# Kernel tuning notes

Measured on AMD Instinct MI355X. Metric: run time of the kernel, lower is better.

Reference implementation:

```python
import jax, jax.numpy as jnp
import numpy as np

N = 262144          # batch size
C = 100             # num_classes
R0, R1 = 0.95, 1.0  # recall_range
LAM = 0.5           # lambda_pauc
LS = 0.1            # label_smoothing
MAX_PAUC = R1 - R0


def setup_inputs() -> dict:
    key = jax.random.key(0)
    k1, k2 = jax.random.split(key)
    predictions = jax.random.normal(k1, (N, C), dtype=jnp.float32)
    targets = jax.random.randint(k2, (N,), 0, C)
    weight = jnp.ones((C,), dtype=jnp.float32)
    return {"predictions": predictions, "targets": targets, "weight": weight}


def _roc_curves(scores, labels):
    """Vectorized per-class ROC. scores, labels: [C, N].
    Replaces the O(N^2) per-threshold loop with sort + cumsum (tie-correct:
    tp at threshold s_j counts ALL samples with score >= s_j)."""
    order = jnp.argsort(-scores, axis=1)                      # descending
    ss = jnp.take_along_axis(scores, order, axis=1)           # [C, N]
    sl = jnp.take_along_axis(labels, order, axis=1)           # [C, N]
    cpos = jnp.cumsum(sl, axis=1)                             # cumulative positives
    # last index within each tie-group of equal scores
    neg = -ss  # ascending
    idx = jax.vmap(lambda a: jnp.searchsorted(a, a, side='right'))(neg) - 1
    tp = jnp.take_along_axis(cpos, idx, axis=1)
    cnt = (idx + 1).astype(scores.dtype)
    fp = cnt - tp
    P = cpos[:, -1:]                       # total positives per class
    Nn = scores.shape[1] - P               # total negatives per class
    tpr = jnp.where(P > 0, tp / jnp.maximum(P, 1.0), 0.0)
    fpr = jnp.where(Nn > 0, fp / jnp.maximum(Nn, 1.0), 0.0)
    return fpr, tpr


def reference(predictions, targets, weight):
    probs = jax.nn.softmax(predictions, axis=1)               # [N, C]
    onehot = jnp.eye(C, dtype=predictions.dtype)[targets]     # [N, C]
    onehot_s = (1.0 - LS) * onehot + LS / C

    # per-class binary labels (smoothed true-class value > 0.5)
    labels = (onehot_s > 0.5).astype(predictions.dtype).T     # [C, N]
    scores = probs.T                                          # [C, N]

    fpr, tpr = _roc_curves(scores, labels)
    mask = (tpr >= R0) & (tpr <= R1)
    y = jnp.maximum(tpr - R0, 0.0)
    # tpr is monotone non-decreasing, so the recall mask is contiguous and
    # trapz over the masked subset == sum over adjacent pairs both in mask.
    pm = (mask[:, :-1] & mask[:, 1:]).astype(predictions.dtype)
    pauc = jnp.sum(0.5 * (y[:, :-1] + y[:, 1:]) * (fpr[:, 1:] - fpr[:, :-1]) * pm, axis=1)  # [C]

    avg_p_auc = jnp.sum(pauc * weight) / (jnp.sum(weight) * MAX_PAUC)
    # torch computes TP/FP via .item(): the pAUC path carries no gradient
    avg_p_auc = jax.lax.stop_gradient(jnp.clip(avg_p_auc, 0.0, 1.0))

    log_probs = jax.nn.log_softmax(predictions, axis=1)
    ce_loss = -jnp.mean(jnp.sum(onehot_s * log_probs * weight, axis=1))
    pauc_loss = 1.0 - avg_p_auc ** 2
    return (1.0 - LAM) * ce_loss + LAM * pauc_loss
```

## Files before the change

kernel.cpp:

```cpp
#include <hip/hip_runtime.h>
#include <math.h>

#define WAVE 64
constexpr int   CC      = 100;
constexpr int   MAXM    = 160;
constexpr int   BUCKET  = 4096;
constexpr int   LCAP    = 4096;
constexpr float LSMOOTH = 0.1f;
constexpr int   TILE    = 64;
constexpr int   ZN      = 3 * CC + 8;

__global__ __launch_bounds__(256) void k1_tile(
    const float* __restrict__ pred, const int* __restrict__ targets,
    const float* __restrict__ weight, float* __restrict__ L_out,
    float* __restrict__ pos_out, float* __restrict__ ce_partial,
    int* __restrict__ zero_blk, int N)
{
    __shared__ float tile[TILE * CC];
    __shared__ int   ttgt[TILE];
    __shared__ float tL[TILE], tpos[TILE];
    __shared__ float cered[4];
    const int tid = threadIdx.x;
    const int r0  = blockIdx.x * TILE;

    if (blockIdx.x == 0)
        for (int i = tid; i < ZN; i += 256) zero_blk[i] = 0;

    const float4* src = (const float4*)(pred + (size_t)r0 * CC);
    #pragma unroll
    for (int t = tid; t < TILE * (CC / 4); t += 256)
        *((float4*)&tile[t * 4]) = src[t];
    if (tid < TILE) ttgt[tid] = targets[r0 + tid];
    __syncthreads();

    const int x = tid & 15;
    const int G = tid >> 4;
    float w[7];
    #pragma unroll
    for (int j = 0; j < 7; ++j) {
        int c = x + 16 * j;
        w[j] = (c < CC) ? weight[c] : 0.0f;
    }
    float Wl = 0.0f;
    #pragma unroll
    for (int j = 0; j < 7; ++j) Wl += w[j];
    #pragma unroll
    for (int off = 1; off < 16; off <<= 1) Wl += __shfl_xor(Wl, off, 16);

    float ce_acc = 0.0f;
    #pragma unroll
    for (int rr = 0; rr < 4; ++rr) {
        const int r = G * 4 + rr;
        const float* rp = tile + r * CC;
        float v[7];
        #pragma unroll
        for (int j = 0; j < 7; ++j) {
            int c = x + 16 * j;
            v[j] = (c < CC) ? rp[c] : -INFINITY;
        }
        float vmax = v[0];
        #pragma unroll
        for (int j = 1; j < 7; ++j) vmax = fmaxf(vmax, v[j]);
        #pragma unroll
        for (int off = 1; off < 16; off <<= 1) vmax = fmaxf(vmax, __shfl_xor(vmax, off, 16));
        float z = 0.0f, ws = 0.0f;
        #pragma unroll
        for (int j = 0; j < 7; ++j) {
            int c = x + 16 * j;
            if (c < CC) { z += __expf(v[j] - vmax); ws += w[j] * v[j]; }
        }
        #pragma unroll
        for (int off = 1; off < 16; off <<= 1) {
            z  += __shfl_xor(z,  off, 16);
            ws += __shfl_xor(ws, off, 16);
        }
        float L = vmax + __logf(z);
        if (x == 0) {
            int t = ttgt[r];
            float pt = rp[t];
            tL[r] = L; tpos[r] = pt - L;
            ce_acc += -((1.0f - LSMOOTH) * weight[t] * (pt - L)
                        + (LSMOOTH / CC) * (ws - Wl * L));
        }
    }
    #pragma unroll
    for (int off = 32; off; off >>= 1) ce_acc += __shfl_xor(ce_acc, off, WAVE);
    if ((tid & 63) == 0) cered[tid >> 6] = ce_acc;
    __syncthreads();
    if (tid < TILE) {
        L_out[r0 + tid]   = tL[tid];
        pos_out[r0 + tid] = tpos[tid];
    }
    if (tid == 0)
        ce_partial[blockIdx.x] = cered[0] + cered[1] + cered[2] + cered[3];
}

__global__ __launch_bounds__(256) void k1b_scatter(
    const int* __restrict__ targets, const float* __restrict__ pos,
    int* __restrict__ cls_cnt, float* __restrict__ bucket, int N)
{
    __shared__ int hist[CC];
    __shared__ int base[CC];
    __shared__ int loc[CC];
    const int tid = threadIdx.x;
    const int rowsPerBlock = N / gridDim.x;
    const int r0 = blockIdx.x * rowsPerBlock;
    const int r1 = r0 + rowsPerBlock;
    for (int c = tid; c < CC; c += blockDim.x) { hist[c] = 0; loc[c] = 0; }
    __syncthreads();
    for (int r = r0 + tid; r < r1; r += blockDim.x)
        atomicAdd(&hist[targets[r]], 1);
    __syncthreads();
    for (int c = tid; c < CC; c += blockDim.x)
        base[c] = (hist[c] > 0) ? atomicAdd(&cls_cnt[c], hist[c]) : 0;
    __syncthreads();
    for (int r = r0 + tid; r < r1; r += blockDim.x) {
        int c = targets[r];
        int idx = base[c] + atomicAdd(&loc[c], 1);
        if (idx < BUCKET) bucket[(size_t)c * BUCKET + idx] = pos[r];
    }
}

__global__ __launch_bounds__(256) void k2_select(
    const float* __restrict__ bucket, const int* __restrict__ cls_cnt,
    float* __restrict__ u, int* __restrict__ m_arr, int* __restrict__ P_arr,
    float* __restrict__ wm_arr)
{
    __shared__ unsigned int keys[BUCKET];
    __shared__ unsigned int hist[256];
    __shared__ unsigned int scan[256];
    __shared__ unsigned int sel[256];
    __shared__ unsigned int s_prefix;
    __shared__ int s_rank;
    __shared__ int cnt_lt;
    const int c   = blockIdx.x;
    const int tid = threadIdx.x;
    const int P = min(cls_cnt[c], BUCKET);
    double Kd = 0.95 * (double)P;
    int kf = (int)floor(Kd);
    int m = P - kf;
    if (m > MAXM) m = MAXM;
    if (m < 0) m = 0;
    if (tid == 0) {
        m_arr[c] = m; P_arr[c] = P;
        wm_arr[c] = (float)((double)(kf + 1) - Kd);
        s_prefix = 0; s_rank = m - 1; cnt_lt = 0;
    }
    for (int i = tid; i < P; i += 256) {
        unsigned int b = __float_as_uint(bucket[(size_t)c * BUCKET + i]);
        keys[i] = (b & 0x80000000u) ? ~b : (b | 0x80000000u);
    }
    __syncthreads();
    if (m == 0) return;

    for (int shift = 24; shift >= 0; shift -= 8) {
        hist[tid] = 0;
        __syncthreads();
        unsigned int pref = s_prefix;
        for (int i = tid; i < P; i += 256) {
            unsigned int k = keys[i];
            bool match = (shift == 24) || ((k >> (shift + 8)) == pref);
            if (match) atomicAdd(&hist[(k >> shift) & 255u], 1u);
        }
        __syncthreads();
        scan[tid] = hist[tid];
        __syncthreads();
        for (int off = 1; off < 256; off <<= 1) {
            unsigned int add = (tid >= off) ? scan[tid - off] : 0u;
            __syncthreads();
            scan[tid] += add;
            __syncthreads();
        }
        int r = s_rank;
        unsigned int inc = scan[tid];
        unsigned int exc = inc - hist[tid];
        __syncthreads();
        if ((unsigned int)r >= exc && (unsigned int)r < inc) {
            s_rank   = r - (int)exc;
            s_prefix = (pref << 8) | (unsigned int)tid;
        }
        __syncthreads();
    }
    const unsigned int kth = s_prefix;

    for (int i = tid; i < P; i += 256) {
        unsigned int k = keys[i];
        if (k < kth) {
            int pslot = atomicAdd(&cnt_lt, 1);
            sel[pslot] = k;
        }
    }
    __syncthreads();
    const int nlt = cnt_lt;
    for (int j = nlt + tid; j < 256; j += 256) sel[j] = (j < m) ? kth : 0xFFFFFFFFu;
    __syncthreads();
    for (int kk = 2; kk <= 256; kk <<= 1) {
        for (int j = kk >> 1; j > 0; j >>= 1) {
            int i = tid, ixj = tid ^ j;
            if (ixj > i) {
                unsigned int a = sel[i], b = sel[ixj];
                bool up = ((i & kk) == 0);
                if ((a > b) == up) { sel[i] = b; sel[ixj] = a; }
            }
            __syncthreads();
        }
    }
    if (tid < m) {
        unsigned int k = sel[tid];
        unsigned int b = (k & 0x80000000u) ? (k & 0x7fffffffu) : ~k;
        u[c * MAXM + tid] = __uint_as_float(b);
    }
}

__device__ __forceinline__ int ubound(const float* uc, int m, float key, int maxidx) {
    int l = 0;
    #pragma unroll
    for (int s = 128; s; s >>= 1) {
        int p = l + s - 1;
        float val = uc[p < maxidx ? p : maxidx];
        l += ((p < m) && (val <= key)) ? s : 0;
    }
    return l;
}

__global__ __launch_bounds__(256) void k3_fused(
    const float4* __restrict__ pred4, const float* __restrict__ L,
    const float* __restrict__ u, const int* __restrict__ m_arr,
    int* __restrict__ g_cnt, int* __restrict__ g_sum, int* __restrict__ done,
    const float* __restrict__ ce_partial, int nPartial,
    const float* __restrict__ weight, const int* __restrict__ P_arr,
    const float* __restrict__ wm_arr, float* __restrict__ out,
    int N, int total4)
{
    __shared__ float umax_s[CC];
    __shared__ int   sm[CC];
    __shared__ int   lcnt[CC], lsum[CC];
    __shared__ uint2 buf[LCAP];
    __shared__ int   lc;
    __shared__ int   isLast;
    __shared__ double r1[256], r2[256], r3[256];
    const int tid = threadIdx.x;
    if (tid < CC) {
        int m = m_arr[tid];
        sm[tid] = m;
        umax_s[tid] = (m > 0) ? u[tid * MAXM + m - 1] : -INFINITY;
        lcnt[tid] = 0; lsum[tid] = 0;
    }
    if (tid == 0) lc = 0;
    __syncthreads();

    const int stride = gridDim.x * blockDim.x;
    int i = blockIdx.x * blockDim.x + tid;
    int j = i % 25;
    int n = i / 25;
    const int dj = stride % 25, dn = stride / 25;
    while (i < total4) {
        float4 v = pred4[i];
        float Ln = L[n];
        float4 um = *((const float4*)&umax_s[j * 4]);
        float s0 = v.x - Ln, s1 = v.y - Ln, s2 = v.z - Ln, s3 = v.w - Ln;
        #pragma unroll
        for (int q = 0; q < 4; ++q) {
            float sc = (q == 0) ? s0 : (q == 1) ? s1 : (q == 2) ? s2 : s3;
            float mx = (q == 0) ? um.x : (q == 1) ? um.y : (q == 2) ? um.z : um.w;
            if (sc < mx) {
                int c = j * 4 + q;
                int idx = atomicAdd(&lc, 1);
                if (idx < LCAP) {
                    buf[idx] = make_uint2((unsigned int)c, __float_as_uint(sc));
                } else {
                    int m = sm[c];
                    int l = ubound(u + c * MAXM, m, sc, MAXM - 1);
                    atomicAdd(&lcnt[c], 1);
                    atomicAdd(&lsum[c], m - 1 - l);
                }
            }
        }
        i += stride; j += dj; n += dn;
        if (j >= 25) { j -= 25; n += 1; }
    }
    __syncthreads();

    const int cnt = min(lc, LCAP);
    for (int k = tid; k < cnt; k += 256) {
        uint2 e = buf[k];
        int c = (int)e.x;
        float key = __uint_as_float(e.y);
        int m = sm[c];
        int l = ubound(u + c * MAXM, m, key, MAXM - 1);
        atomicAdd(&lcnt[c], 1);
        atomicAdd(&lsum[c], m - 1 - l);
    }
    __syncthreads();
    for (int c = tid; c < CC; c += 256) {
        if (lcnt[c]) { atomicAdd(&g_cnt[c], lcnt[c]); atomicAdd(&g_sum[c], lsum[c]); }
    }

    if (tid == 0) {
        __threadfence();
        int t = atomicAdd(done, 1);
        isLast = (t == (int)gridDim.x - 1);
    }
    __syncthreads();
    if (!isLast) return;
    __threadfence();

    double ce = 0.0;
    for (int k = tid; k < nPartial; k += 256) ce += (double)ce_partial[k];
    double p = 0.0, wsum = 0.0;
    for (int c = tid; c < CC; c += 256) {
        int P = P_arr[c], m = sm[c];
        double wgt = (double)weight[c];
        long long Nn = (long long)N - P;
        if (P > 0 && Nn > 0 && m > 0) {
            double wm = (double)wm_arr[c];
            double S   = (double)atomicAdd(&g_sum[c], 0)
                       + wm * (double)atomicAdd(&g_cnt[c], 0);
            double sub = 0.5 * (double)(m - 1) * (double)(m - 2) + wm * (double)(m - 1);
            double pc  = (S - sub) / ((double)Nn * (double)P);
            if (pc < 0.0) pc = 0.0;
            p += pc * wgt;
        }
        wsum += wgt;
    }
    r1[tid] = ce; r2[tid] = p; r3[tid] = wsum;
    __syncthreads();
    for (int off = 128; off; off >>= 1) {
        if (tid < off) {
            r1[tid] += r1[tid + off];
            r2[tid] += r2[tid + off];
            r3[tid] += r3[tid + off];
        }
        __syncthreads();
    }
    if (tid == 0) {
        double ce_loss = r1[0] / (double)N;
        double avg = r2[0] / (r3[0] * 0.05);
        avg = fmin(fmax(avg, 0.0), 1.0);
        out[0] = (float)(0.5 * ce_loss + 0.5 * (1.0 - avg * avg));
    }
}

extern "C" void kernel_launch(void* const* d_in, const int* in_sizes, int n_in,
                              void* d_out, int out_size, void* d_ws, size_t ws_size,
                              hipStream_t stream) {
    (void)n_in; (void)out_size; (void)ws_size;
    const float* pred    = (const float*)d_in[0];
    const int*   targets = (const int*)d_in[1];
    const float* weight  = (const float*)d_in[2];
    float* out = (float*)d_out;
    const int N = in_sizes[1];

    const int K1_BLOCKS = N / TILE;
    char* base = (char*)d_ws;
    size_t off = 0;
    auto take = [&](size_t bytes) { char* q = base + off; off += (bytes + 15) & ~(size_t)15; return q; };
    float* L_ws       = (float*)take((size_t)N * 4);
    float* pos_ws     = (float*)take((size_t)N * 4);
    float* ce_partial = (float*)take((size_t)K1_BLOCKS * 4);
    float* u          = (float*)take((size_t)CC * MAXM * 4);
    int*   m_arr      = (int*)take(CC * 4);
    int*   P_arr      = (int*)take(CC * 4);
    float* wm_arr     = (float*)take(CC * 4);
    int*   zero_blk   = (int*)take(ZN * 4);
    int*   cls_cnt  = zero_blk;
    int*   g_cnt    = zero_blk + CC;
    int*   g_sum    = zero_blk + 2 * CC;
    int*   done     = zero_blk + 3 * CC;
    float* bucket     = (float*)take((size_t)CC * BUCKET * 4);

    k1_tile<<<K1_BLOCKS, 256, 0, stream>>>(pred, targets, weight, L_ws, pos_ws,
                                           ce_partial, zero_blk, N);
    k1b_scatter<<<256, 256, 0, stream>>>(targets, pos_ws, cls_cnt, bucket, N);
    k2_select<<<CC, 256, 0, stream>>>(bucket, cls_cnt, u, m_arr, P_arr, wm_arr);
    const int total4 = (int)((size_t)N * CC / 4);
    k3_fused<<<1024, 256, 0, stream>>>((const float4*)pred, L_ws, u, m_arr,
                                       g_cnt, g_sum, done, ce_partial, K1_BLOCKS,
                                       weight, P_arr, wm_arr, out, N, total4);
}
```

Baseline: 265.5 us.

## Reduce k3 per-block pAUC partials directly and double grid with smaller LDS buffer

Each k3 block now computes its weighted pAUC contribution locally and writes one double partial to a per-block slot, instead of atomically adding per-class counts into global counters. The last block sums the partials and subtracts a per-class correction term. The double reduction arrays now reuse the candidate buffer, and LCAP is halved, which shrinks shared memory per block; the grid doubles to 2048 blocks so more blocks can be resident. This trades fewer global atomics and better occupancy against a larger final reduction and a greater chance of overflowing the smaller per-block candidate buffer.

Result: no change. 267.2 us (+0.6%).

```diff
diff --git a/kernel.cpp b/kernel.cpp
--- a/kernel.cpp
+++ b/kernel.cpp
@@ -5,10 +5,11 @@
 constexpr int   CC      = 100;
 constexpr int   MAXM    = 160;
 constexpr int   BUCKET  = 4096;
-constexpr int   LCAP    = 4096;
+constexpr int   LCAP    = 2048;
 constexpr float LSMOOTH = 0.1f;
 constexpr int   TILE    = 64;
-constexpr int   ZN      = 3 * CC + 8;
+constexpr int   ZN      = CC + 8;
+constexpr int   K3_BLOCKS = 2048;
 
 __global__ __launch_bounds__(256) void k1_tile(
     const float* __restrict__ pred, const int* __restrict__ targets,
@@ -226,23 +227,27 @@
 __global__ __launch_bounds__(256) void k3_fused(
     const float4* __restrict__ pred4, const float* __restrict__ L,
     const float* __restrict__ u, const int* __restrict__ m_arr,
-    int* __restrict__ g_cnt, int* __restrict__ g_sum, int* __restrict__ done,
+    const int* __restrict__ P_arr, const float* __restrict__ wm_arr,
+    const float* __restrict__ weight,
+    unsigned long long* __restrict__ partial_p, int* __restrict__ done,
     const float* __restrict__ ce_partial, int nPartial,
-    const float* __restrict__ weight, const int* __restrict__ P_arr,
-    const float* __restrict__ wm_arr, float* __restrict__ out,
-    int N, int total4)
+    float* __restrict__ out, int N, int total4)
 {
     __shared__ float umax_s[CC];
     __shared__ int   sm[CC];
+    __shared__ int   sP[CC];
+    __shared__ float swm[CC], swgt[CC];
     __shared__ int   lcnt[CC], lsum[CC];
     __shared__ uint2 buf[LCAP];
     __shared__ int   lc;
     __shared__ int   isLast;
-    __shared__ double r1[256], r2[256], r3[256];
     const int tid = threadIdx.x;
     if (tid < CC) {
         int m = m_arr[tid];
-        sm[tid] = m;
+        sm[tid]  = m;
+        sP[tid]  = P_arr[tid];
+        swm[tid] = wm_arr[tid];
+        swgt[tid] = weight[tid];
         umax_s[tid] = (m > 0) ? u[tid * MAXM + m - 1] : -INFINITY;
         lcnt[tid] = 0; lsum[tid] = 0;
     }
@@ -292,9 +297,25 @@
         atomicAdd(&lsum[c], m - 1 - l);
     }
     __syncthreads();
-    for (int c = tid; c < CC; c += 256) {
-        if (lcnt[c]) { atomicAdd(&g_cnt[c], lcnt[c]); atomicAdd(&g_sum[c], lsum[c]); }
-    }
+
+    double part = 0.0;
+    if (tid < CC) {
+        int P = sP[tid], m = sm[tid];
+        if (P > 0 && P < N && m > 0) {
+            part = (double)swgt[tid]
+                 * ((double)lsum[tid] + (double)swm[tid] * (double)lcnt[tid])
+                 / ((double)(N - P) * (double)P);
+        }
+    }
+    double* red = (double*)buf;
+    red[tid] = part;
+    __syncthreads();
+    for (int off = 128; off; off >>= 1) {
+        if (tid < off) red[tid] += red[tid + off];
+        __syncthreads();
+    }
+    if (tid == 0)
+        atomicExch(&partial_p[blockIdx.x], (unsigned long long)__double_as_longlong(red[0]));
 
     if (tid == 0) {
         __threadfence();
@@ -305,37 +326,41 @@
     if (!isLast) return;
     __threadfence();
 
+    double psum = 0.0;
+    for (int b = tid; b < (int)gridDim.x; b += 256)
+        psum += __longlong_as_double((long long)atomicAdd(&partial_p[b], 0ull));
     double ce = 0.0;
     for (int k = tid; k < nPartial; k += 256) ce += (double)ce_partial[k];
-    double p = 0.0, wsum = 0.0;
-    for (int c = tid; c < CC; c += 256) {
-        int P = P_arr[c], m = sm[c];
-        double wgt = (double)weight[c];
-        long long Nn = (long long)N - P;
-        if (P > 0 && Nn > 0 && m > 0) {
-            double wm = (double)wm_arr[c];
-            double S   = (double)atomicAdd(&g_sum[c], 0)
-                       + wm * (double)atomicAdd(&g_cnt[c], 0);
-            double sub = 0.5 * (double)(m - 1) * (double)(m - 2) + wm * (double)(m - 1);
-            double pc  = (S - sub) / ((double)Nn * (double)P);
-            if (pc < 0.0) pc = 0.0;
-            p += pc * wgt;
-        }
-        wsum += wgt;
-    }
-    r1[tid] = ce; r2[tid] = p; r3[tid] = wsum;
+    double sub = 0.0, wsum = 0.0;
+    if (tid < CC) {
+        wsum = (double)swgt[tid];
+        int P = sP[tid], m = sm[tid];
+        if (P > 0 && P < N && m > 0) {
+            double wm = (double)swm[tid];
+            sub = (double)swgt[tid]
+                * (0.5 * (double)(m - 1) * (double)(m - 2) + wm * (double)(m - 1))
+                / ((double)(N - P) * (double)P);
+        }
+    }
+    __syncthreads();
+    double* r1 = red; double* r2 = red + 256;
+    r1[tid] = ce; r2[tid] = psum - sub;
     __syncthreads();
     for (int off = 128; off; off >>= 1) {
-        if (tid < off) {
-            r1[tid] += r1[tid + off];
-            r2[tid] += r2[tid + off];
-            r3[tid] += r3[tid + off];
-        }
+        if (tid < off) { r1[tid] += r1[tid + off]; r2[tid] += r2[tid + off]; }
+        __syncthreads();
+    }
+    double ce_tot = r1[0], p_tot = r2[0];
+    __syncthreads();
+    r1[tid] = wsum;
+    __syncthreads();
+    for (int off = 128; off; off >>= 1) {
+        if (tid < off) r1[tid] += r1[tid + off];
         __syncthreads();
     }
     if (tid == 0) {
-        double ce_loss = r1[0] / (double)N;
-        double avg = r2[0] / (r3[0] * 0.05);
+        double ce_loss = ce_tot / (double)N;
+        double avg = p_tot / (r1[0] * 0.05);
         avg = fmin(fmax(avg, 0.0), 1.0);
         out[0] = (float)(0.5 * ce_loss + 0.5 * (1.0 - avg * avg));
     }
@@ -364,9 +389,8 @@
     float* wm_arr     = (float*)take(CC * 4);
     int*   zero_blk   = (int*)take(ZN * 4);
     int*   cls_cnt  = zero_blk;
-    int*   g_cnt    = zero_blk + CC;
-    int*   g_sum    = zero_blk + 2 * CC;
-    int*   done     = zero_blk + 3 * CC;
+    int*   done     = zero_blk + CC;
+    unsigned long long* partial_p = (unsigned long long*)take((size_t)K3_BLOCKS * 8);
     float* bucket     = (float*)take((size_t)CC * BUCKET * 4);
 
     k1_tile<<<K1_BLOCKS, 256, 0, stream>>>(pred, targets, weight, L_ws, pos_ws,
@@ -374,7 +398,7 @@
     k1b_scatter<<<256, 256, 0, stream>>>(targets, pos_ws, cls_cnt, bucket, N);
     k2_select<<<CC, 256, 0, stream>>>(bucket, cls_cnt, u, m_arr, P_arr, wm_arr);
     const int total4 = (int)((size_t)N * CC / 4);
-    k3_fused<<<1024, 256, 0, stream>>>((const float4*)pred, L_ws, u, m_arr,
-                                       g_cnt, g_sum, done, ce_partial, K1_BLOCKS,
-                                       weight, P_arr, wm_arr, out, N, total4);
-}
+    k3_fused<<<K3_BLOCKS, 256, 0, stream>>>((const float4*)pred, L_ws, u, m_arr,
+                                            P_arr, wm_arr, weight, partial_p, done,
+                                            ce_partial, K1_BLOCKS, out, N, total4);
+}
```
